# Kernel optimization log

Hardware: AMD Instinct MI355X
Metric: run time of the kernel (lower is better)

## Reference

```python
import jax, jax.numpy as jnp
import numpy as np

EPS = 1e-5

def _ln(t, w, b):
    m = t.mean(-1, keepdims=True)
    xc = t - m
    var = (xc * xc).mean(-1, keepdims=True)
    return xc * jax.lax.rsqrt(var + EPS) * w + b

def _rope(q, k, cos, sin):
    # q,k: [B,H,N,hd]; cos,sin: [N, hd//2]
    def rot(t):
        B, H, N, hd = t.shape
        tp = t.reshape(B, H, N, hd // 2, 2)
        r, i = tp[..., 0], tp[..., 1]
        c = cos[None, None, :, :]
        s = sin[None, None, :, :]
        orr = r * c - i * s
        oii = r * s + i * c
        return jnp.stack([orr, oii], axis=-1).reshape(B, H, N, hd)
    return rot(q), rot(k)

def setup_inputs() -> dict:
    key = jax.random.key(0)
    B, N1, N2, D, H = 2, 2048, 256, 1024, 16
    hd = D // H
    ks = jax.random.split(key, 8)
    def w(k, shape):
        return jax.random.normal(k, shape, jnp.float32) * 0.02
    x = jax.random.normal(ks[0], (B, N1, D), jnp.float32)
    c = jax.random.normal(ks[1], (B, N2, D), jnp.float32)
    # rotary tables
    t = jnp.arange(N1, dtype=jnp.float32)
    inv_freq = 1.0 / (10000.0 ** (jnp.arange(0, hd, 2, dtype=jnp.float32) / hd))
    ang = jnp.outer(t, inv_freq)  # [N1, hd//2]
    return dict(
        x=x, c=c,
        freqs_cos=jnp.cos(ang), freqs_sin=jnp.sin(ang),
        W_qkv1=w(ks[2], (D, 3 * D)), b_qkv1=jnp.zeros(3 * D, jnp.float32),
        W_qkv2=w(ks[3], (D, 3 * D)), b_qkv2=jnp.zeros(3 * D, jnp.float32),
        qn1_w=jnp.ones(hd, jnp.float32), qn1_b=jnp.zeros(hd, jnp.float32),
        kn1_w=jnp.ones(hd, jnp.float32), kn1_b=jnp.zeros(hd, jnp.float32),
        qn2_w=jnp.ones(hd, jnp.float32), qn2_b=jnp.zeros(hd, jnp.float32),
        kn2_w=jnp.ones(hd, jnp.float32), kn2_b=jnp.zeros(hd, jnp.float32),
        W_proj1=w(ks[4], (D, D)), b_proj1=jnp.zeros(D, jnp.float32),
        W_proj2=w(ks[5], (D, D)), b_proj2=jnp.zeros(D, jnp.float32),
        pre_x=0,
    )

def reference(x, c, freqs_cos, freqs_sin,
              W_qkv1, b_qkv1, W_qkv2, b_qkv2,
              qn1_w, qn1_b, kn1_w, kn1_b,
              qn2_w, qn2_b, kn2_w, kn2_b,
              W_proj1, b_proj1, W_proj2, b_proj2, pre_x):
    B, N1, D = x.shape
    N2 = c.shape[1]
    H = 16
    hd = D // H
    scale = hd ** -0.5

    def split_heads(qkv):
        q, k, v = jnp.split(qkv, 3, axis=-1)
        f = lambda t: t.reshape(B, -1, H, hd).transpose(0, 2, 1, 3)
        return f(q), f(k), f(v)

    q1, k1, v1 = split_heads(x @ W_qkv1 + b_qkv1)
    q1 = _ln(q1, qn1_w, qn1_b)
    k1 = _ln(k1, kn1_w, kn1_b)
    if pre_x:
        qr, kr = _rope(q1[:, :, pre_x:], k1[:, :, pre_x:], freqs_cos, freqs_sin)
        q1 = jnp.concatenate([q1[:, :, :pre_x], qr], axis=2)
        k1 = jnp.concatenate([k1[:, :, :pre_x], kr], axis=2)
    else:
        q1, k1 = _rope(q1, k1, freqs_cos, freqs_sin)

    q2, k2, v2 = split_heads(c @ W_qkv2 + b_qkv2)
    q2 = _ln(q2, qn2_w, qn2_b)
    k2 = _ln(k2, kn2_w, kn2_b)

    q = jnp.concatenate([q1, q2], axis=2)
    k = jnp.concatenate([k1, k2], axis=2)
    v = jnp.concatenate([v1, v2], axis=2)

    scores = jnp.einsum('bhqd,bhkd->bhqk', q, k) * scale
    attn = jax.nn.softmax(scores, axis=-1)
    o = jnp.einsum('bhqk,bhkd->bhqd', attn, v)  # [B,H,N,hd]
    o = o.transpose(0, 2, 1, 3).reshape(B, N1 + N2, D)

    x_out = o[:, :N1] @ W_proj1 + b_proj1
    c_out = o[:, N1:] @ W_proj2 + b_proj2
    return (x_out, c_out)
```

## Files before the change

kernel.cpp:

```cpp
#include <hip/hip_runtime.h>
#include <hip/hip_bf16.h>
#include <stdint.h>

typedef __attribute__((ext_vector_type(8))) short short8;
typedef __attribute__((ext_vector_type(4))) short bf4;
typedef __attribute__((ext_vector_type(4))) float f32x4;

#define B_ 2
#define N1 2048
#define N2 256
#define NT 2304
#define D_ 1024
#define H_ 16
#define HD 64
#define QSCALE 0.18033688011112042f
#define RESCALE_THR 8.0f

static __device__ __forceinline__ float bf2f(short s){
  union { unsigned int u; float f; } u;
  u.u = ((unsigned int)(unsigned short)s) << 16;
  return u.f;
}
static __device__ __forceinline__ short f2bf(float f){
  union { float f; unsigned int u; } v; v.f = f;
  unsigned int u = v.u;
  unsigned int lsb = (u >> 16) & 1u;
  u += 0x7fffu + lsb;
  return (short)(u >> 16);
}
static __device__ __forceinline__ unsigned int cvtpk2(float a, float b){
  union { __hip_bfloat162 h; unsigned int u; } cv;
  cv.h = __float22bfloat162_rn(make_float2(a, b));
  return cv.u;
}

static __device__ __forceinline__ float fexp2(float x){
#if __has_builtin(__builtin_amdgcn_exp2f)
  return __builtin_amdgcn_exp2f(x);
#else
  return exp2f(x);
#endif
}

static __device__ __forceinline__ void gload16(const void* g, void* l){
  __builtin_amdgcn_global_load_lds(
      (const __attribute__((address_space(1))) void*)g,
      (__attribute__((address_space(3))) void*)l, 16, 0, 0);
}

static __device__ __forceinline__ int swz(int row, int chunk){
  return (row << 6) + ((chunk ^ (row & 7)) << 3);
}

__global__ __launch_bounds__(256) void k_cvt_all(const float* __restrict__ x,
                                                 const float* __restrict__ c,
                                                 short* __restrict__ out){
  int i = (blockIdx.x * 256 + threadIdx.x) * 8;
  const float* in = (i < 4194304) ? (x + i) : (c + (i - 4194304));
  float4 a = *(const float4*)(in);
  float4 b = *(const float4*)(in + 4);
  short8 o;
  o[0]=f2bf(a.x); o[1]=f2bf(a.y); o[2]=f2bf(a.z); o[3]=f2bf(a.w);
  o[4]=f2bf(b.x); o[5]=f2bf(b.y); o[6]=f2bf(b.z); o[7]=f2bf(b.w);
  *(short8*)(out + i) = o;
}

__global__ __launch_bounds__(256) void k_transpose_w4(
    const float* __restrict__ Wq1, const float* __restrict__ Wq2,
    const float* __restrict__ Wp1, const float* __restrict__ Wp2,
    short* __restrict__ Wt1, short* __restrict__ Wt2,
    short* __restrict__ Wtp1, short* __restrict__ Wtp2){
  const int id = blockIdx.x;
  const float* W; short* Wt; int N; int bx, by;
  if (id < 768)      { W = Wq1; Wt = Wt1;  N = 3072; bx = id % 48;          by = id / 48; }
  else if (id < 1536){ W = Wq2; Wt = Wt2;  N = 3072; bx = (id-768) % 48;    by = (id-768) / 48; }
  else if (id < 1792){ W = Wp1; Wt = Wtp1; N = 1024; bx = (id-1536) % 16;   by = (id-1536) / 16; }
  else               { W = Wp2; Wt = Wtp2; N = 1024; bx = (id-1792) % 16;   by = (id-1792) / 16; }
  const int K = 1024;
  __shared__ float tl[64][65];
  const int n0 = bx * 64, k0 = by * 64;
  const int t = threadIdx.x, r = t >> 2, c = (t & 3) * 16;
  const float* src = W + (size_t)(k0 + r) * N + n0 + c;
  #pragma unroll
  for (int i = 0; i < 16; i += 4){
    float4 v = *(const float4*)(src + i);
    tl[r][c+i] = v.x; tl[r][c+i+1] = v.y; tl[r][c+i+2] = v.z; tl[r][c+i+3] = v.w;
  }
  __syncthreads();
  short8 o0, o1;
  #pragma unroll
  for (int i = 0; i < 8; i++) o0[i] = f2bf(tl[c+i][r]);
  #pragma unroll
  for (int i = 0; i < 8; i++) o1[i] = f2bf(tl[c+8+i][r]);
  short* dst = Wt + (size_t)(n0 + r) * K + k0 + c;
  *(short8*)(dst)     = o0;
  *(short8*)(dst + 8) = o1;
}

__global__ __launch_bounds__(256) void k_gemm_qkv(const short* __restrict__ A,
    const short* __restrict__ Bt, const short* __restrict__ Bt2,
    const float* __restrict__ bias, const float* __restrict__ bias2,
    const float* __restrict__ qn1w, const float* __restrict__ qn1b,
    const float* __restrict__ kn1w, const float* __restrict__ kn1b,
    const float* __restrict__ qn2w, const float* __restrict__ qn2b,
    const float* __restrict__ kn2w, const float* __restrict__ kn2b,
    const float* __restrict__ fcos, const float* __restrict__ fsin,
    short* __restrict__ Qo, short* __restrict__ Ko, short* __restrict__ Vto){
  __shared__ __align__(16) short As[128*32];
  __shared__ __align__(16) short Bs[128*32];
  const int t = threadIdx.x;
  const int w = t >> 6, l = t & 63;
  const int lc = l & 15, g = l >> 4;
  const int gx = gridDim.x;
  const int nb = gx * gridDim.y;
  const int bid = blockIdx.y * gx + blockIdx.x;
  const int nbid = (bid & 7) * (nb >> 3) + (bid >> 3);
  const int tm = (nbid / gx) * 128, tn = (nbid % gx) * 128;
  const int wm = (w >> 1) * 64, wn = (w & 1) * 64;
  const int K = 1024;
  const bool s1 = (tm < 4096);

  const short* Bsel = s1 ? Bt : Bt2;
  const float* bsel = s1 ? bias : bias2;

  const int r0 = w*32 + (l >> 2);
  const int r1 = r0 + 16;
  const int cb = (l & 3) * 16;

  const char* Ag0 = (const char*)(A + (size_t)(tm + r0) * K) + cb;
  const char* Ag1 = (const char*)(A + (size_t)(tm + r1) * K) + cb;
  const char* Bg0 = (const char*)(Bsel + (size_t)(tn + r0) * K) + cb;
  const char* Bg1 = (const char*)(Bsel + (size_t)(tn + r1) * K) + cb;
  char* Al0 = (char*)As + (w*2  )*1024;
  char* Al1 = (char*)As + (w*2+1)*1024;
  char* Bl0 = (char*)Bs + (w*2  )*1024;
  char* Bl1 = (char*)Bs + (w*2+1)*1024;

  f32x4 acc[4][4];
  #pragma unroll
  for (int m=0;m<4;m++){
    #pragma unroll
    for (int n=0;n<4;n++){ acc[m][n][0]=0.f; acc[m][n][1]=0.f; acc[m][n][2]=0.f; acc[m][n][3]=0.f; }
  }

  for (int k0 = 0; k0 < K; k0 += 32){
    const int kb = k0 * 2;
    gload16(Ag0 + kb, Al0);
    gload16(Ag1 + kb, Al1);
    gload16(Bg0 + kb, Bl0);
    gload16(Bg1 + kb, Bl1);
    __syncthreads();
    short8 af[4], bfr[4];
    #pragma unroll
    for (int m=0;m<4;m++) af[m]  = *(const short8*)(As + (wm + m*16 + lc)*32 + g*8);
    #pragma unroll
    for (int n=0;n<4;n++) bfr[n] = *(const short8*)(Bs + (wn + n*16 + lc)*32 + g*8);
    #pragma unroll
    for (int m=0;m<4;m++){
      #pragma unroll
      for (int n=0;n<4;n++)
        acc[m][n] = __builtin_amdgcn_mfma_f32_16x16x32_bf16(af[m], bfr[n], acc[m][n], 0, 0, 0);
    }
    __syncthreads();
  }

  #pragma unroll
  for (int n=0;n<4;n++){
    const float bv = bsel[tn + wn + n*16 + lc];
    #pragma unroll
    for (int m=0;m<4;m++){
      acc[m][n][0] += bv; acc[m][n][1] += bv; acc[m][n][2] += bv; acc[m][n][3] += bv;
    }
  }

  const int colbase = tn + wn;
  const int grp = colbase >> 10;
  const int hh = (colbase & 1023) >> 6;

  if (grp == 2){
    #pragma unroll
    for (int m=0;m<4;m++){
      const int row0 = tm + wm + m*16 + g*4;
      const int bb  = s1 ? (row0 >> 11) : ((row0 - 4096) >> 8);
      const int pos = s1 ? (row0 & 2047) : (2048 + ((row0 - 4096) & 255));
      short* vbase = Vto + (size_t)(bb*16 + hh) * 64 * NT + pos;
      #pragma unroll
      for (int n=0;n<4;n++){
        const int d = n*16 + lc;
        bf4 ov;
        #pragma unroll
        for (int r=0;r<4;r++) ov[r] = f2bf(acc[m][n][r]);
        *(bf4*)(vbase + (size_t)d * NT) = ov;
      }
    }
    return;
  }

  const float* lnw = (grp == 0) ? (s1 ? qn1w : qn2w) : (s1 ? kn1w : kn2w);
  const float* lnb = (grp == 0) ? (s1 ? qn1b : qn2b) : (s1 ? kn1b : kn2b);
  short* outp = (grp == 0) ? Qo : Ko;
  float wv_[4], bv_[4];
  #pragma unroll
  for (int n=0;n<4;n++){ wv_[n] = lnw[n*16 + lc]; bv_[n] = lnb[n*16 + lc]; }

  #pragma unroll
  for (int m=0;m<4;m++){
    float mu[4], rv[4];
    #pragma unroll
    for (int r=0;r<4;r++){
      float s  = (acc[m][0][r] + acc[m][1][r]) + (acc[m][2][r] + acc[m][3][r]);
      float sq = (acc[m][0][r]*acc[m][0][r] + acc[m][1][r]*acc[m][1][r])
               + (acc[m][2][r]*acc[m][2][r] + acc[m][3][r]*acc[m][3][r]);
      s  += __shfl_xor(s, 1, 64);  sq += __shfl_xor(sq, 1, 64);
      s  += __shfl_xor(s, 2, 64);  sq += __shfl_xor(sq, 2, 64);
      s  += __shfl_xor(s, 4, 64);  sq += __shfl_xor(sq, 4, 64);
      s  += __shfl_xor(s, 8, 64);  sq += __shfl_xor(sq, 8, 64);
      mu[r] = s * (1.f/64.f);
      const float var = sq * (1.f/64.f) - mu[r]*mu[r];
      rv[r] = rsqrtf(var + 1e-5f);
    }
    const int row0 = tm + wm + m*16 + g*4;
    const int bb  = s1 ? (row0 >> 11) : ((row0 - 4096) >> 8);
    const int pos0 = s1 ? (row0 & 2047) : (2048 + ((row0 - 4096) & 255));
    short* obase = outp + ((size_t)(bb*16 + hh) * NT + pos0) * 64;
    #pragma unroll
    for (int n=0;n<4;n++){
      float xh[4];
      #pragma unroll
      for (int r=0;r<4;r++) xh[r] = (acc[m][n][r] - mu[r]) * rv[r] * wv_[n] + bv_[n];
      if (s1){
        #pragma unroll
        for (int r=0;r<4;r++){
          const size_t fi = (size_t)(pos0 + r) * 32 + n*8 + (lc >> 1);
          const float cv = fcos[fi];
          const float sv = fsin[fi];
          const float p = __shfl_xor(xh[r], 1, 64);
          xh[r] = (lc & 1) ? (p*sv + xh[r]*cv) : (xh[r]*cv - p*sv);
        }
      }
      if (grp == 0){
        #pragma unroll
        for (int r=0;r<4;r++) xh[r] *= QSCALE;
      }
      const int d = n*16 + lc;
      #pragma unroll
      for (int r=0;r<4;r++) obase[(size_t)r * 64 + d] = f2bf(xh[r]);
    }
  }
}

__global__ __launch_bounds__(256) void k_gemm_proj(const short* __restrict__ A,
                                                   const short* __restrict__ Bt,
                                                   const short* __restrict__ Bt2,
                                                   const float* __restrict__ bias,
                                                   const float* __restrict__ bias2,
                                                   float* __restrict__ Cp,
                                                   int N, int K, int Msplit){
  __shared__ __align__(16) short As[128*32];
  __shared__ __align__(16) short Bs[128*32];
  const int t = threadIdx.x;
  const int w = t >> 6, l = t & 63;
  const int lc = l & 15, g = l >> 4;
  const int gx = gridDim.x;
  const int nb = gx * gridDim.y;
  const int bid = blockIdx.y * gx + blockIdx.x;
  const int nbid = (bid & 7) * (nb >> 3) + (bid >> 3);
  const int tm = (nbid / gx) * 128, tn = (nbid % gx) * 128;
  const int wm = (w >> 1) * 64, wn = (w & 1) * 64;

  const short* Bsel = (tm < Msplit) ? Bt : Bt2;
  const float* bsel = (tm < Msplit) ? bias : bias2;

  const int r0 = w*32 + (l >> 2);
  const int r1 = r0 + 16;
  const int cb = (l & 3) * 16;

  const char* Ag0 = (const char*)(A + (size_t)(tm + r0) * K) + cb;
  const char* Ag1 = (const char*)(A + (size_t)(tm + r1) * K) + cb;
  const char* Bg0 = (const char*)(Bsel + (size_t)(tn + r0) * K) + cb;
  const char* Bg1 = (const char*)(Bsel + (size_t)(tn + r1) * K) + cb;
  char* Al0 = (char*)As + (w*2  )*1024;
  char* Al1 = (char*)As + (w*2+1)*1024;
  char* Bl0 = (char*)Bs + (w*2  )*1024;
  char* Bl1 = (char*)Bs + (w*2+1)*1024;

  f32x4 acc[4][4];
  #pragma unroll
  for (int m=0;m<4;m++){
    #pragma unroll
    for (int n=0;n<4;n++){ acc[m][n][0]=0.f; acc[m][n][1]=0.f; acc[m][n][2]=0.f; acc[m][n][3]=0.f; }
  }

  for (int k0 = 0; k0 < K; k0 += 32){
    const int kb = k0 * 2;
    gload16(Ag0 + kb, Al0);
    gload16(Ag1 + kb, Al1);
    gload16(Bg0 + kb, Bl0);
    gload16(Bg1 + kb, Bl1);
    __syncthreads();
    short8 af[4], bfr[4];
    #pragma unroll
    for (int m=0;m<4;m++) af[m]  = *(const short8*)(As + (wm + m*16 + lc)*32 + g*8);
    #pragma unroll
    for (int n=0;n<4;n++) bfr[n] = *(const short8*)(Bs + (wn + n*16 + lc)*32 + g*8);
    #pragma unroll
    for (int m=0;m<4;m++){
      #pragma unroll
      for (int n=0;n<4;n++)
        acc[m][n] = __builtin_amdgcn_mfma_f32_16x16x32_bf16(af[m], bfr[n], acc[m][n], 0, 0, 0);
    }
    __syncthreads();
  }

  #pragma unroll
  for (int n=0;n<4;n++){
    const int col = tn + wn + n*16 + lc;
    const float bv = bsel[col];
    #pragma unroll
    for (int m=0;m<4;m++){
      const int row = tm + wm + m*16 + g*4;
      #pragma unroll
      for (int r=0;r<4;r++)
        Cp[(size_t)(row + r)*N + col] = acc[m][n][r] + bv;
    }
  }
}

__global__ __launch_bounds__(512) void k_attn(const short* __restrict__ Q,
                                              const short* __restrict__ Kg,
                                              const short* __restrict__ Vt,
                                              short* __restrict__ o1,
                                              short* __restrict__ o2){
  __shared__ __align__(16) short Kl[2][4096];
  __shared__ __align__(16) short Vl[2][4096];
  __shared__ __align__(16) short Ps[8][1024];
  const int t = threadIdx.x, w = t >> 6, l = t & 63;
  const int lc = l & 15, g = l >> 4;
  const int blk = blockIdx.x;
  const int ch = blk & 7, ii = blk >> 3;
  const int bh = ch * 4 + (ii / 18);
  const int qt = ii % 18;
  const int b = bh >> 4, hh = bh & 15;
  const int q0 = qt * 128 + w * 16;
  const short* Qb = Q  + (size_t)bh * NT * HD;
  const short* Kb = Kg + (size_t)bh * NT * HD;
  const short* Vb = Vt + (size_t)bh * HD * NT;

  short8 qf0 = *(const short8*)(Qb + (size_t)(q0 + lc) * HD + g*8);
  short8 qf1 = *(const short8*)(Qb + (size_t)(q0 + lc) * HD + g*8 + 32);

  const int sr = t >> 3, c0 = t & 7;
  const short* Kgp = Kb + (size_t)sr * HD + c0 * 8;
  const short* Vgp = Vb + (size_t)sr * NT + c0 * 8;
  const int w0 = swz(sr, c0);

  float mcur = -1e30f, lcur = 0.f;
  f32x4 oacc[4];
  #pragma unroll
  for (int j=0;j<4;j++){ oacc[j][0]=0.f; oacc[j][1]=0.f; oacc[j][2]=0.f; oacc[j][3]=0.f; }

  {
    short8 k0 = *(const short8*)(Kgp);
    short8 v0 = *(const short8*)(Vgp);
    *(short8*)&Kl[0][w0] = k0;
    *(short8*)&Vl[0][w0] = v0;
  }
  __syncthreads();

  for (int ti = 0; ti < 36; ++ti){
    const int cur = ti & 1;
    short8 kn0, vn0;
    if (ti < 35){
      kn0 = *(const short8*)(Kgp + (size_t)(ti + 1) * 64 * HD);
      vn0 = *(const short8*)(Vgp + (ti + 1) * 64);
    }
    f32x4 s[4];
    __builtin_amdgcn_s_setprio(1);
    #pragma unroll
    for (int j=0;j<4;j++){
      const int row = j*16 + lc;
      short8 k0 = *(const short8*)(&Kl[cur][swz(row, g)]);
      short8 k1 = *(const short8*)(&Kl[cur][swz(row, g + 4)]);
      f32x4 a; a[0]=0.f; a[1]=0.f; a[2]=0.f; a[3]=0.f;
      a = __builtin_amdgcn_mfma_f32_16x16x32_bf16(k0, qf0, a, 0, 0, 0);
      a = __builtin_amdgcn_mfma_f32_16x16x32_bf16(k1, qf1, a, 0, 0, 0);
      s[j] = a;
    }
    __builtin_amdgcn_s_setprio(0);
    float t0 = fmaxf(fmaxf(s[0][0], s[0][1]), fmaxf(s[0][2], s[0][3]));
    float t1 = fmaxf(fmaxf(s[1][0], s[1][1]), fmaxf(s[1][2], s[1][3]));
    float t2 = fmaxf(fmaxf(s[2][0], s[2][1]), fmaxf(s[2][2], s[2][3]));
    float t3 = fmaxf(fmaxf(s[3][0], s[3][1]), fmaxf(s[3][2], s[3][3]));
    float tmx = fmaxf(fmaxf(t0, t1), fmaxf(t2, t3));
    tmx = fmaxf(tmx, __shfl_xor(tmx, 16, 64));
    tmx = fmaxf(tmx, __shfl_xor(tmx, 32, 64));
    float mn = mcur;
    if (__any(tmx > mcur + RESCALE_THR)){
      mn = fmaxf(mcur, tmx);
      const float fsc = fexp2(mcur - mn);
      mcur = mn;
      lcur *= fsc;
      #pragma unroll
      for (int j=0;j<4;j++){
        oacc[j][0] *= fsc; oacc[j][1] *= fsc; oacc[j][2] *= fsc; oacc[j][3] *= fsc;
      }
    }
    float p[4][4];
    #pragma unroll
    for (int j=0;j<4;j++){
      p[j][0] = fexp2(s[j][0] - mn);
      p[j][1] = fexp2(s[j][1] - mn);
      p[j][2] = fexp2(s[j][2] - mn);
      p[j][3] = fexp2(s[j][3] - mn);
    }
    float rs = ((p[0][0]+p[0][1])+(p[0][2]+p[0][3]))
             + ((p[1][0]+p[1][1])+(p[1][2]+p[1][3]))
             + ((p[2][0]+p[2][1])+(p[2][2]+p[2][3]))
             + ((p[3][0]+p[3][1])+(p[3][2]+p[3][3]));
    rs += __shfl_xor(rs, 16, 64);
    rs += __shfl_xor(rs, 32, 64);
    lcur += rs;
    #pragma unroll
    for (int j=0;j<4;j++){
      const int si = (lc << 6) + (((2*j + (g >> 1)) ^ (lc & 7)) << 3) + (g & 1) * 4;
      unsigned int* dst = (unsigned int*)&Ps[w][si];
      dst[0] = cvtpk2(p[j][0], p[j][1]);
      dst[1] = cvtpk2(p[j][2], p[j][3]);
    }
    #pragma unroll
    for (int kk=0;kk<2;kk++){
      short8 pa = *(const short8*)(&Ps[w][swz(lc, 4*kk + g)]);
      __builtin_amdgcn_s_setprio(1);
      #pragma unroll
      for (int jd=0;jd<4;jd++){
        short8 vb = *(const short8*)(&Vl[cur][swz(lc + 16*jd, 4*kk + g)]);
        oacc[jd] = __builtin_amdgcn_mfma_f32_16x16x32_bf16(vb, pa, oacc[jd], 0, 0, 0);
      }
      __builtin_amdgcn_s_setprio(0);
    }
    if (ti < 35){
      *(short8*)&Kl[cur ^ 1][w0] = kn0;
      *(short8*)&Vl[cur ^ 1][w0] = vn0;
    }
    __syncthreads();
  }

  const float inv = 1.0f / lcur;
  const int qi = q0 + lc;
  short* obase = (qi < N1) ? (o1 + ((size_t)b * N1 + qi) * D_)
                           : (o2 + ((size_t)b * N2 + (qi - N1)) * D_);
  #pragma unroll
  for (int jd=0;jd<4;jd++){
    bf4 ov;
    #pragma unroll
    for (int r=0;r<4;r++) ov[r] = f2bf(oacc[jd][r] * inv);
    *(bf4*)(obase + hh*64 + 16*jd + 4*g) = ov;
  }
}

extern "C" void kernel_launch(void* const* d_in, const int* in_sizes, int n_in,
                              void* d_out, int out_size, void* d_ws, size_t ws_size,
                              hipStream_t stream){
  const float* x    = (const float*)d_in[0];
  const float* c    = (const float*)d_in[1];
  const float* fc   = (const float*)d_in[2];
  const float* fs   = (const float*)d_in[3];
  const float* Wq1  = (const float*)d_in[4];
  const float* bq1  = (const float*)d_in[5];
  const float* Wq2  = (const float*)d_in[6];
  const float* bq2  = (const float*)d_in[7];
  const float* qn1w = (const float*)d_in[8];
  const float* qn1b = (const float*)d_in[9];
  const float* kn1w = (const float*)d_in[10];
  const float* kn1b = (const float*)d_in[11];
  const float* qn2w = (const float*)d_in[12];
  const float* qn2b = (const float*)d_in[13];
  const float* kn2w = (const float*)d_in[14];
  const float* kn2b = (const float*)d_in[15];
  const float* Wp1  = (const float*)d_in[16];
  const float* bp1  = (const float*)d_in[17];
  const float* Wp2  = (const float*)d_in[18];
  const float* bp2  = (const float*)d_in[19];
  float* out = (float*)d_out;

  char* ws = (char*)d_ws;
  short* xb   = (short*)(ws);
  short* Wt1  = (short*)(ws + 9437184);
  short* Wt2  = (short*)(ws + 15728640);
  short* Wtp1 = (short*)(ws + 22020096);
  short* Wtp2 = (short*)(ws + 24117248);
  short* o1   = (short*)(ws + 26214400);
  short* Vtb  = (short*)(ws + 26214400 + 9437184);
  short* Qb   = (short*)(ws + 54525952);
  short* Kb   = (short*)(ws + 63963136);

  k_cvt_all<<<2304, 256, 0, stream>>>(x, c, xb);
  k_transpose_w4<<<2048, 256, 0, stream>>>(Wq1, Wq2, Wp1, Wp2, Wt1, Wt2, Wtp1, Wtp2);

  k_gemm_qkv<<<dim3(24,36), 256, 0, stream>>>(xb, Wt1, Wt2, bq1, bq2,
      qn1w, qn1b, kn1w, kn1b, qn2w, qn2b, kn2w, kn2b, fc, fs, Qb, Kb, Vtb);

  k_attn<<<576, 512, 0, stream>>>(Qb, Kb, Vtb, o1, o1 + 4194304);

  k_gemm_proj<<<dim3(8,36), 256, 0, stream>>>(o1, Wtp1, Wtp2, bp1, bp2, out, 1024, 1024, 4096);
}
```

Measured before the change: 189.4 us.

## Process two query tiles per warp in attention with 256-thread blocks

Attention blocks drop from 8 to 4 warps, and each warp now handles two 16-row query tiles against the same K/V fragments. Each K and V fragment read from shared memory feeds two MFMAs, which halves LDS reads per unit of compute and adds independent work per warp. The cost is roughly double the accumulator and softmax registers per thread and fewer waves per block, which may lower occupancy and latency hiding.

```diff
diff --git a/kernel.cpp b/kernel.cpp
--- a/kernel.cpp
+++ b/kernel.cpp
@@ -326,14 +326,14 @@
   }
 }
 
-__global__ __launch_bounds__(512) void k_attn(const short* __restrict__ Q,
+__global__ __launch_bounds__(256) void k_attn(const short* __restrict__ Q,
                                               const short* __restrict__ Kg,
                                               const short* __restrict__ Vt,
                                               short* __restrict__ o1,
                                               short* __restrict__ o2){
   __shared__ __align__(16) short Kl[2][4096];
   __shared__ __align__(16) short Vl[2][4096];
-  __shared__ __align__(16) short Ps[8][1024];
+  __shared__ __align__(16) short Ps[4][2][1024];
   const int t = threadIdx.x, w = t >> 6, l = t & 63;
   const int lc = l & 15, g = l >> 4;
   const int blk = blockIdx.x;
@@ -346,35 +346,48 @@
   const short* Kb = Kg + (size_t)bh * NT * HD;
   const short* Vb = Vt + (size_t)bh * HD * NT;
 
-  short8 qf0 = *(const short8*)(Qb + (size_t)(q0 + lc) * HD + g*8);
-  short8 qf1 = *(const short8*)(Qb + (size_t)(q0 + lc) * HD + g*8 + 32);
-
-  const int sr = t >> 3, c0 = t & 7;
+  short8 qA0 = *(const short8*)(Qb + (size_t)(q0 + lc) * HD + g*8);
+  short8 qA1 = *(const short8*)(Qb + (size_t)(q0 + lc) * HD + g*8 + 32);
+  short8 qB0 = *(const short8*)(Qb + (size_t)(q0 + 64 + lc) * HD + g*8);
+  short8 qB1 = *(const short8*)(Qb + (size_t)(q0 + 64 + lc) * HD + g*8 + 32);
+
+  const int sr = t >> 2, c0 = (t & 3) * 2;
   const short* Kgp = Kb + (size_t)sr * HD + c0 * 8;
   const short* Vgp = Vb + (size_t)sr * NT + c0 * 8;
-  const int w0 = swz(sr, c0);
-
-  float mcur = -1e30f, lcur = 0.f;
-  f32x4 oacc[4];
-  #pragma unroll
-  for (int j=0;j<4;j++){ oacc[j][0]=0.f; oacc[j][1]=0.f; oacc[j][2]=0.f; oacc[j][3]=0.f; }
+  const int w0 = swz(sr, c0), w1 = swz(sr, c0 + 1);
+
+  float mA = -1e30f, lA = 0.f, mB = -1e30f, lB = 0.f;
+  f32x4 oA[4], oB[4];
+  #pragma unroll
+  for (int j=0;j<4;j++){
+    oA[j][0]=0.f; oA[j][1]=0.f; oA[j][2]=0.f; oA[j][3]=0.f;
+    oB[j][0]=0.f; oB[j][1]=0.f; oB[j][2]=0.f; oB[j][3]=0.f;
+  }
 
   {
     short8 k0 = *(const short8*)(Kgp);
+    short8 k1 = *(const short8*)(Kgp + 8);
     short8 v0 = *(const short8*)(Vgp);
+    short8 v1 = *(const short8*)(Vgp + 8);
     *(short8*)&Kl[0][w0] = k0;
+    *(short8*)&Kl[0][w1] = k1;
     *(short8*)&Vl[0][w0] = v0;
+    *(short8*)&Vl[0][w1] = v1;
   }
   __syncthreads();
 
   for (int ti = 0; ti < 36; ++ti){
     const int cur = ti & 1;
-    short8 kn0, vn0;
+    short8 kn0, kn1, vn0, vn1;
     if (ti < 35){
-      kn0 = *(const short8*)(Kgp + (size_t)(ti + 1) * 64 * HD);
-      vn0 = *(const short8*)(Vgp + (ti + 1) * 64);
-    }
-    f32x4 s[4];
+      const short* kp = Kgp + (size_t)(ti + 1) * 64 * HD;
+      const short* vp = Vgp + (ti + 1) * 64;
+      kn0 = *(const short8*)(kp);
+      kn1 = *(const short8*)(kp + 8);
+      vn0 = *(const short8*)(vp);
+      vn1 = *(const short8*)(vp + 8);
+    }
+    f32x4 sA[4], sB[4];
     __builtin_amdgcn_s_setprio(1);
     #pragma unroll
     for (int j=0;j<4;j++){
@@ -382,79 +395,147 @@
       short8 k0 = *(const short8*)(&Kl[cur][swz(row, g)]);
       short8 k1 = *(const short8*)(&Kl[cur][swz(row, g + 4)]);
       f32x4 a; a[0]=0.f; a[1]=0.f; a[2]=0.f; a[3]=0.f;
-      a = __builtin_amdgcn_mfma_f32_16x16x32_bf16(k0, qf0, a, 0, 0, 0);
-      a = __builtin_amdgcn_mfma_f32_16x16x32_bf16(k1, qf1, a, 0, 0, 0);
-      s[j] = a;
+      a = __builtin_amdgcn_mfma_f32_16x16x32_bf16(k0, qA0, a, 0, 0, 0);
+      a = __builtin_amdgcn_mfma_f32_16x16x32_bf16(k1, qA1, a, 0, 0, 0);
+      sA[j] = a;
+      f32x4 bb; bb[0]=0.f; bb[1]=0.f; bb[2]=0.f; bb[3]=0.f;
+      bb = __builtin_amdgcn_mfma_f32_16x16x32_bf16(k0, qB0, bb, 0, 0, 0);
+      bb = __builtin_amdgcn_mfma_f32_16x16x32_bf16(k1, qB1, bb, 0, 0, 0);
+      sB[j] = bb;
     }
     __builtin_amdgcn_s_setprio(0);
-    float t0 = fmaxf(fmaxf(s[0][0], s[0][1]), fmaxf(s[0][2], s[0][3]));
-    float t1 = fmaxf(fmaxf(s[1][0], s[1][1]), fmaxf(s[1][2], s[1][3]));
-    float t2 = fmaxf(fmaxf(s[2][0], s[2][1]), fmaxf(s[2][2], s[2][3]));
-    float t3 = fmaxf(fmaxf(s[3][0], s[3][1]), fmaxf(s[3][2], s[3][3]));
-    float tmx = fmaxf(fmaxf(t0, t1), fmaxf(t2, t3));
-    tmx = fmaxf(tmx, __shfl_xor(tmx, 16, 64));
-    tmx = fmaxf(tmx, __shfl_xor(tmx, 32, 64));
-    float mn = mcur;
-    if (__any(tmx > mcur + RESCALE_THR)){
-      mn = fmaxf(mcur, tmx);
-      const float fsc = fexp2(mcur - mn);
-      mcur = mn;
-      lcur *= fsc;
+
+    {
+      float t0 = fmaxf(fmaxf(sA[0][0], sA[0][1]), fmaxf(sA[0][2], sA[0][3]));
+      float t1 = fmaxf(fmaxf(sA[1][0], sA[1][1]), fmaxf(sA[1][2], sA[1][3]));
+      float t2 = fmaxf(fmaxf(sA[2][0], sA[2][1]), fmaxf(sA[2][2], sA[2][3]));
+      float t3 = fmaxf(fmaxf(sA[3][0], sA[3][1]), fmaxf(sA[3][2], sA[3][3]));
+      float tmx = fmaxf(fmaxf(t0, t1), fmaxf(t2, t3));
+      tmx = fmaxf(tmx, __shfl_xor(tmx, 16, 64));
+      tmx = fmaxf(tmx, __shfl_xor(tmx, 32, 64));
+      float mn = mA;
+      if (__any(tmx > mA + RESCALE_THR)){
+        mn = fmaxf(mA, tmx);
+        const float fsc = fexp2(mA - mn);
+        mA = mn;
+        lA *= fsc;
+        #pragma unroll
+        for (int j=0;j<4;j++){
+          oA[j][0] *= fsc; oA[j][1] *= fsc; oA[j][2] *= fsc; oA[j][3] *= fsc;
+        }
+      }
+      float p[4][4];
       #pragma unroll
       for (int j=0;j<4;j++){
-        oacc[j][0] *= fsc; oacc[j][1] *= fsc; oacc[j][2] *= fsc; oacc[j][3] *= fsc;
-      }
-    }
-    float p[4][4];
-    #pragma unroll
-    for (int j=0;j<4;j++){
-      p[j][0] = fexp2(s[j][0] - mn);
-      p[j][1] = fexp2(s[j][1] - mn);
-      p[j][2] = fexp2(s[j][2] - mn);
-      p[j][3] = fexp2(s[j][3] - mn);
-    }
-    float rs = ((p[0][0]+p[0][1])+(p[0][2]+p[0][3]))
-             + ((p[1][0]+p[1][1])+(p[1][2]+p[1][3]))
-             + ((p[2][0]+p[2][1])+(p[2][2]+p[2][3]))
-             + ((p[3][0]+p[3][1])+(p[3][2]+p[3][3]));
-    rs += __shfl_xor(rs, 16, 64);
-    rs += __shfl_xor(rs, 32, 64);
-    lcur += rs;
-    #pragma unroll
-    for (int j=0;j<4;j++){
-      const int si = (lc << 6) + (((2*j + (g >> 1)) ^ (lc & 7)) << 3) + (g & 1) * 4;
-      unsigned int* dst = (unsigned int*)&Ps[w][si];
-      dst[0] = cvtpk2(p[j][0], p[j][1]);
-      dst[1] = cvtpk2(p[j][2], p[j][3]);
+        p[j][0] = fexp2(sA[j][0] - mn);
+        p[j][1] = fexp2(sA[j][1] - mn);
+        p[j][2] = fexp2(sA[j][2] - mn);
+        p[j][3] = fexp2(sA[j][3] - mn);
+      }
+      float rs = ((p[0][0]+p[0][1])+(p[0][2]+p[0][3]))
+               + ((p[1][0]+p[1][1])+(p[1][2]+p[1][3]))
+               + ((p[2][0]+p[2][1])+(p[2][2]+p[2][3]))
+               + ((p[3][0]+p[3][1])+(p[3][2]+p[3][3]));
+      rs += __shfl_xor(rs, 16, 64);
+      rs += __shfl_xor(rs, 32, 64);
+      lA += rs;
+      #pragma unroll
+      for (int j=0;j<4;j++){
+        const int si = (lc << 6) + (((2*j + (g >> 1)) ^ (lc & 7)) << 3) + (g & 1) * 4;
+        unsigned int* dst = (unsigned int*)&Ps[w][0][si];
+        dst[0] = cvtpk2(p[j][0], p[j][1]);
+        dst[1] = cvtpk2(p[j][2], p[j][3]);
+      }
+    }
+    {
+      float t0 = fmaxf(fmaxf(sB[0][0], sB[0][1]), fmaxf(sB[0][2], sB[0][3]));
+      float t1 = fmaxf(fmaxf(sB[1][0], sB[1][1]), fmaxf(sB[1][2], sB[1][3]));
+      float t2 = fmaxf(fmaxf(sB[2][0], sB[2][1]), fmaxf(sB[2][2], sB[2][3]));
+      float t3 = fmaxf(fmaxf(sB[3][0], sB[3][1]), fmaxf(sB[3][2], sB[3][3]));
+      float tmx = fmaxf(fmaxf(t0, t1), fmaxf(t2, t3));
+      tmx = fmaxf(tmx, __shfl_xor(tmx, 16, 64));
+      tmx = fmaxf(tmx, __shfl_xor(tmx, 32, 64));
+      float mn = mB;
+      if (__any(tmx > mB + RESCALE_THR)){
+        mn = fmaxf(mB, tmx);
+        const float fsc = fexp2(mB - mn);
+        mB = mn;
+        lB *= fsc;
+        #pragma unroll
+        for (int j=0;j<4;j++){
+          oB[j][0] *= fsc; oB[j][1] *= fsc; oB[j][2] *= fsc; oB[j][3] *= fsc;
+        }
+      }
+      float p[4][4];
+      #pragma unroll
+      for (int j=0;j<4;j++){
+        p[j][0] = fexp2(sB[j][0] - mn);
+        p[j][1] = fexp2(sB[j][1] - mn);
+        p[j][2] = fexp2(sB[j][2] - mn);
+        p[j][3] = fexp2(sB[j][3] - mn);
+      }
+      float rs = ((p[0][0]+p[0][1])+(p[0][2]+p[0][3]))
+               + ((p[1][0]+p[1][1])+(p[1][2]+p[1][3]))
+               + ((p[2][0]+p[2][1])+(p[2][2]+p[2][3]))
+               + ((p[3][0]+p[3][1])+(p[3][2]+p[3][3]));
+      rs += __shfl_xor(rs, 16, 64);
+      rs += __shfl_xor(rs, 32, 64);
+      lB += rs;
+      #pragma unroll
+      for (int j=0;j<4;j++){
+        const int si = (lc << 6) + (((2*j + (g >> 1)) ^ (lc & 7)) << 3) + (g & 1) * 4;
+        unsigned int* dst = (unsigned int*)&Ps[w][1][si];
+        dst[0] = cvtpk2(p[j][0], p[j][1]);
+        dst[1] = cvtpk2(p[j][2], p[j][3]);
+      }
     }
     #pragma unroll
     for (int kk=0;kk<2;kk++){
-      short8 pa = *(const short8*)(&Ps[w][swz(lc, 4*kk + g)]);
+      short8 paA = *(const short8*)(&Ps[w][0][swz(lc, 4*kk + g)]);
+      short8 paB = *(const short8*)(&Ps[w][1][swz(lc, 4*kk + g)]);
       __builtin_amdgcn_s_setprio(1);
       #pragma unroll
       for (int jd=0;jd<4;jd++){
         short8 vb = *(const short8*)(&Vl[cur][swz(lc + 16*jd, 4*kk + g)]);
-        oacc[jd] = __builtin_amdgcn_mfma_f32_16x16x32_bf16(vb, pa, oacc[jd], 0, 0, 0);
+        oA[jd] = __builtin_amdgcn_mfma_f32_16x16x32_bf16(vb, paA, oA[jd], 0, 0, 0);
+        oB[jd] = __builtin_amdgcn_mfma_f32_16x16x32_bf16(vb, paB, oB[jd], 0, 0, 0);
       }
       __builtin_amdgcn_s_setprio(0);
     }
     if (ti < 35){
       *(short8*)&Kl[cur ^ 1][w0] = kn0;
+      *(short8*)&Kl[cur ^ 1][w1] = kn1;
       *(short8*)&Vl[cur ^ 1][w0] = vn0;
+      *(short8*)&Vl[cur ^ 1][w1] = vn1;
     }
     __syncthreads();
   }
 
-  const float inv = 1.0f / lcur;
-  const int qi = q0 + lc;
-  short* obase = (qi < N1) ? (o1 + ((size_t)b * N1 + qi) * D_)
-                           : (o2 + ((size_t)b * N2 + (qi - N1)) * D_);
-  #pragma unroll
-  for (int jd=0;jd<4;jd++){
-    bf4 ov;
-    #pragma unroll
-    for (int r=0;r<4;r++) ov[r] = f2bf(oacc[jd][r] * inv);
-    *(bf4*)(obase + hh*64 + 16*jd + 4*g) = ov;
+  {
+    const float inv = 1.0f / lA;
+    const int qi = q0 + lc;
+    short* obase = (qi < N1) ? (o1 + ((size_t)b * N1 + qi) * D_)
+                             : (o2 + ((size_t)b * N2 + (qi - N1)) * D_);
+    #pragma unroll
+    for (int jd=0;jd<4;jd++){
+      bf4 ov;
+      #pragma unroll
+      for (int r=0;r<4;r++) ov[r] = f2bf(oA[jd][r] * inv);
+      *(bf4*)(obase + hh*64 + 16*jd + 4*g) = ov;
+    }
+  }
+  {
+    const float inv = 1.0f / lB;
+    const int qi = q0 + 64 + lc;
+    short* obase = (qi < N1) ? (o1 + ((size_t)b * N1 + qi) * D_)
+                             : (o2 + ((size_t)b * N2 + (qi - N1)) * D_);
+    #pragma unroll
+    for (int jd=0;jd<4;jd++){
+      bf4 ov;
+      #pragma unroll
+      for (int r=0;r<4;r++) ov[r] = f2bf(oB[jd][r] * inv);
+      *(bf4*)(obase + hh*64 + 16*jd + 4*g) = ov;
+    }
   }
 }
 
@@ -500,7 +581,7 @@
   k_gemm_qkv<<<dim3(24,36), 256, 0, stream>>>(xb, Wt1, Wt2, bq1, bq2,
       qn1w, qn1b, kn1w, kn1b, qn2w, qn2b, kn2w, kn2b, fc, fs, Qb, Kb, Vtb);
 
-  k_attn<<<576, 512, 0, stream>>>(Qb, Kb, Vtb, o1, o1 + 4194304);
+  k_attn<<<576, 256, 0, stream>>>(Qb, Kb, Vtb, o1, o1 + 4194304);
 
   k_gemm_proj<<<dim3(8,36), 256, 0, stream>>>(o1, Wtp1, Wtp2, bp1, bp2, out, 1024, 1024, 4096);
 }
```

New measurement: 218.4 us. 1.15x slower.

## Rework attention kernel around 32x32 MFMA with register-resident P and direct LDS loads

Applied to the files above, without the earlier changes.

Rewrites the attention kernel to run 4 waves of 32 query rows each, using 32x32x16 bf16 MFMA for both QK^T and PV. The softmax probabilities stay in registers and are reshuffled across the two wave halves with lane shuffles, which removes the per-wave LDS staging buffer. K and V tiles now go straight from global memory into LDS through pre-swizzled global_load_lds, and the swizzle function gains an extra XOR term. The intent is to cut LDS traffic, shuffle and reduction work per tile and to raise MFMA efficiency. In exchange each thread holds more accumulator registers and the block has half as many threads.

```diff
diff --git a/kernel.cpp b/kernel.cpp
--- a/kernel.cpp
+++ b/kernel.cpp
@@ -5,6 +5,7 @@
 typedef __attribute__((ext_vector_type(8))) short short8;
 typedef __attribute__((ext_vector_type(4))) short bf4;
 typedef __attribute__((ext_vector_type(4))) float f32x4;
+typedef __attribute__((ext_vector_type(16))) float f32x16;
 
 #define B_ 2
 #define N1 2048
@@ -49,7 +50,7 @@
 }
 
 static __device__ __forceinline__ int swz(int row, int chunk){
-  return (row << 6) + ((chunk ^ (row & 7)) << 3);
+  return (row << 6) + (((chunk ^ (row & 7) ^ ((row >> 3) & 7)) & 7) << 3);
 }
 
 __global__ __launch_bounds__(256) void k_cvt_all(const float* __restrict__ x,
@@ -326,73 +327,85 @@
   }
 }
 
-__global__ __launch_bounds__(512) void k_attn(const short* __restrict__ Q,
+__global__ __launch_bounds__(256) void k_attn(const short* __restrict__ Q,
                                               const short* __restrict__ Kg,
                                               const short* __restrict__ Vt,
                                               short* __restrict__ o1,
                                               short* __restrict__ o2){
   __shared__ __align__(16) short Kl[2][4096];
   __shared__ __align__(16) short Vl[2][4096];
-  __shared__ __align__(16) short Ps[8][1024];
   const int t = threadIdx.x, w = t >> 6, l = t & 63;
-  const int lc = l & 15, g = l >> 4;
+  const int q32 = l & 31, h5 = l >> 5;
   const int blk = blockIdx.x;
   const int ch = blk & 7, ii = blk >> 3;
   const int bh = ch * 4 + (ii / 18);
   const int qt = ii % 18;
   const int b = bh >> 4, hh = bh & 15;
-  const int q0 = qt * 128 + w * 16;
+  const int qrow = qt*128 + w*32 + q32;
   const short* Qb = Q  + (size_t)bh * NT * HD;
   const short* Kb = Kg + (size_t)bh * NT * HD;
   const short* Vb = Vt + (size_t)bh * HD * NT;
 
-  short8 qf0 = *(const short8*)(Qb + (size_t)(q0 + lc) * HD + g*8);
-  short8 qf1 = *(const short8*)(Qb + (size_t)(q0 + lc) * HD + g*8 + 32);
-
-  const int sr = t >> 3, c0 = t & 7;
-  const short* Kgp = Kb + (size_t)sr * HD + c0 * 8;
-  const short* Vgp = Vb + (size_t)sr * NT + c0 * 8;
-  const int w0 = swz(sr, c0);
+  short8 qf[4];
+  #pragma unroll
+  for (int hk=0;hk<4;hk++)
+    qf[hk] = *(const short8*)(Qb + (size_t)qrow * HD + hk*16 + h5*8);
+
+  const int srow0 = w*16 + (l >> 3);
+  const int srow1 = srow0 + 8;
+  const int cg0 = (l & 7) ^ (srow0 & 7) ^ ((srow0 >> 3) & 7);
+  const int cg1 = (l & 7) ^ (srow1 & 7) ^ ((srow1 >> 3) & 7);
+  const short* Kg0 = Kb + (size_t)srow0 * HD + cg0*8;
+  const short* Kg1 = Kb + (size_t)srow1 * HD + cg1*8;
+  const short* Vg0 = Vb + (size_t)srow0 * NT + cg0*8;
+  const short* Vg1 = Vb + (size_t)srow1 * NT + cg1*8;
+  const int ld0 = w*1024, ld1 = w*1024 + 512;
 
   float mcur = -1e30f, lcur = 0.f;
-  f32x4 oacc[4];
-  #pragma unroll
-  for (int j=0;j<4;j++){ oacc[j][0]=0.f; oacc[j][1]=0.f; oacc[j][2]=0.f; oacc[j][3]=0.f; }
-
-  {
-    short8 k0 = *(const short8*)(Kgp);
-    short8 v0 = *(const short8*)(Vgp);
-    *(short8*)&Kl[0][w0] = k0;
-    *(short8*)&Vl[0][w0] = v0;
-  }
+  f32x16 oacc[2];
+  #pragma unroll
+  for (int db=0;db<2;db++){
+    #pragma unroll
+    for (int r=0;r<16;r++) oacc[db][r] = 0.f;
+  }
+
+  gload16(Kg0, (char*)&Kl[0][ld0]);
+  gload16(Kg1, (char*)&Kl[0][ld1]);
+  gload16(Vg0, (char*)&Vl[0][ld0]);
+  gload16(Vg1, (char*)&Vl[0][ld1]);
   __syncthreads();
 
-  for (int ti = 0; ti < 36; ++ti){
-    const int cur = ti & 1;
-    short8 kn0, vn0;
-    if (ti < 35){
-      kn0 = *(const short8*)(Kgp + (size_t)(ti + 1) * 64 * HD);
-      vn0 = *(const short8*)(Vgp + (ti + 1) * 64);
-    }
-    f32x4 s[4];
+  for (int pi = 0; pi < 36; ++pi){
+    const int cur = pi & 1;
+    if (pi < 35){
+      const size_t ko = (size_t)(pi + 1) * 64 * HD;
+      const int vo = (pi + 1) * 64;
+      gload16(Kg0 + ko, (char*)&Kl[cur ^ 1][ld0]);
+      gload16(Kg1 + ko, (char*)&Kl[cur ^ 1][ld1]);
+      gload16(Vg0 + vo, (char*)&Vl[cur ^ 1][ld0]);
+      gload16(Vg1 + vo, (char*)&Vl[cur ^ 1][ld1]);
+    }
+    f32x16 s[2];
     __builtin_amdgcn_s_setprio(1);
     #pragma unroll
-    for (int j=0;j<4;j++){
-      const int row = j*16 + lc;
-      short8 k0 = *(const short8*)(&Kl[cur][swz(row, g)]);
-      short8 k1 = *(const short8*)(&Kl[cur][swz(row, g + 4)]);
-      f32x4 a; a[0]=0.f; a[1]=0.f; a[2]=0.f; a[3]=0.f;
-      a = __builtin_amdgcn_mfma_f32_16x16x32_bf16(k0, qf0, a, 0, 0, 0);
-      a = __builtin_amdgcn_mfma_f32_16x16x32_bf16(k1, qf1, a, 0, 0, 0);
-      s[j] = a;
+    for (int kvb=0;kvb<2;kvb++){
+      f32x16 a;
+      #pragma unroll
+      for (int r=0;r<16;r++) a[r] = 0.f;
+      #pragma unroll
+      for (int hk=0;hk<4;hk++){
+        short8 kf = *(const short8*)(&Kl[cur][swz(kvb*32 + q32, hk*2 + h5)]);
+        a = __builtin_amdgcn_mfma_f32_32x32x16_bf16(kf, qf[hk], a, 0, 0, 0);
+      }
+      s[kvb] = a;
     }
     __builtin_amdgcn_s_setprio(0);
-    float t0 = fmaxf(fmaxf(s[0][0], s[0][1]), fmaxf(s[0][2], s[0][3]));
-    float t1 = fmaxf(fmaxf(s[1][0], s[1][1]), fmaxf(s[1][2], s[1][3]));
-    float t2 = fmaxf(fmaxf(s[2][0], s[2][1]), fmaxf(s[2][2], s[2][3]));
-    float t3 = fmaxf(fmaxf(s[3][0], s[3][1]), fmaxf(s[3][2], s[3][3]));
-    float tmx = fmaxf(fmaxf(t0, t1), fmaxf(t2, t3));
-    tmx = fmaxf(tmx, __shfl_xor(tmx, 16, 64));
+    float tmx = -1e30f;
+    #pragma unroll
+    for (int kvb=0;kvb<2;kvb++){
+      #pragma unroll
+      for (int r=0;r<16;r++) tmx = fmaxf(tmx, s[kvb][r]);
+    }
     tmx = fmaxf(tmx, __shfl_xor(tmx, 32, 64));
     float mn = mcur;
     if (__any(tmx > mcur + RESCALE_THR)){
@@ -401,60 +414,62 @@
       mcur = mn;
       lcur *= fsc;
       #pragma unroll
-      for (int j=0;j<4;j++){
-        oacc[j][0] *= fsc; oacc[j][1] *= fsc; oacc[j][2] *= fsc; oacc[j][3] *= fsc;
-      }
-    }
-    float p[4][4];
-    #pragma unroll
-    for (int j=0;j<4;j++){
-      p[j][0] = fexp2(s[j][0] - mn);
-      p[j][1] = fexp2(s[j][1] - mn);
-      p[j][2] = fexp2(s[j][2] - mn);
-      p[j][3] = fexp2(s[j][3] - mn);
-    }
-    float rs = ((p[0][0]+p[0][1])+(p[0][2]+p[0][3]))
-             + ((p[1][0]+p[1][1])+(p[1][2]+p[1][3]))
-             + ((p[2][0]+p[2][1])+(p[2][2]+p[2][3]))
-             + ((p[3][0]+p[3][1])+(p[3][2]+p[3][3]));
-    rs += __shfl_xor(rs, 16, 64);
+      for (int db=0;db<2;db++){
+        #pragma unroll
+        for (int r=0;r<16;r++) oacc[db][r] *= fsc;
+      }
+    }
+    float rs = 0.f;
+    #pragma unroll
+    for (int kvb=0;kvb<2;kvb++){
+      #pragma unroll
+      for (int r=0;r<16;r++){
+        s[kvb][r] = fexp2(s[kvb][r] - mn);
+        rs += s[kvb][r];
+      }
+    }
     rs += __shfl_xor(rs, 32, 64);
     lcur += rs;
     #pragma unroll
-    for (int j=0;j<4;j++){
-      const int si = (lc << 6) + (((2*j + (g >> 1)) ^ (lc & 7)) << 3) + (g & 1) * 4;
-      unsigned int* dst = (unsigned int*)&Ps[w][si];
-      dst[0] = cvtpk2(p[j][0], p[j][1]);
-      dst[1] = cvtpk2(p[j][2], p[j][3]);
-    }
-    #pragma unroll
-    for (int kk=0;kk<2;kk++){
-      short8 pa = *(const short8*)(&Ps[w][swz(lc, 4*kk + g)]);
+    for (int kvs=0;kvs<4;kvs++){
+      const int kvb = kvs >> 1, sb = kvs & 1;
+      const unsigned int A0 = cvtpk2(s[kvb][8*sb+0], s[kvb][8*sb+1]);
+      const unsigned int A1 = cvtpk2(s[kvb][8*sb+2], s[kvb][8*sb+3]);
+      const unsigned int B0 = cvtpk2(s[kvb][8*sb+4], s[kvb][8*sb+5]);
+      const unsigned int B1 = cvtpk2(s[kvb][8*sb+6], s[kvb][8*sb+7]);
+      const unsigned int X0 = (unsigned int)__shfl_xor((int)A0, 32, 64);
+      const unsigned int X1 = (unsigned int)__shfl_xor((int)A1, 32, 64);
+      const unsigned int Y0 = (unsigned int)__shfl_xor((int)B0, 32, 64);
+      const unsigned int Y1 = (unsigned int)__shfl_xor((int)B1, 32, 64);
+      union { unsigned int u[4]; short8 s8; } pf;
+      pf.u[0] = h5 ? Y0 : A0;
+      pf.u[1] = h5 ? Y1 : A1;
+      pf.u[2] = h5 ? B0 : X0;
+      pf.u[3] = h5 ? B1 : X1;
       __builtin_amdgcn_s_setprio(1);
       #pragma unroll
-      for (int jd=0;jd<4;jd++){
-        short8 vb = *(const short8*)(&Vl[cur][swz(lc + 16*jd, 4*kk + g)]);
-        oacc[jd] = __builtin_amdgcn_mfma_f32_16x16x32_bf16(vb, pa, oacc[jd], 0, 0, 0);
+      for (int db=0;db<2;db++){
+        short8 vf = *(const short8*)(&Vl[cur][swz(db*32 + q32, kvs*2 + h5)]);
+        oacc[db] = __builtin_amdgcn_mfma_f32_32x32x16_bf16(vf, pf.s8, oacc[db], 0, 0, 0);
       }
       __builtin_amdgcn_s_setprio(0);
     }
-    if (ti < 35){
-      *(short8*)&Kl[cur ^ 1][w0] = kn0;
-      *(short8*)&Vl[cur ^ 1][w0] = vn0;
-    }
     __syncthreads();
   }
 
   const float inv = 1.0f / lcur;
-  const int qi = q0 + lc;
+  const int qi = qrow;
   short* obase = (qi < N1) ? (o1 + ((size_t)b * N1 + qi) * D_)
                            : (o2 + ((size_t)b * N2 + (qi - N1)) * D_);
   #pragma unroll
-  for (int jd=0;jd<4;jd++){
-    bf4 ov;
-    #pragma unroll
-    for (int r=0;r<4;r++) ov[r] = f2bf(oacc[jd][r] * inv);
-    *(bf4*)(obase + hh*64 + 16*jd + 4*g) = ov;
+  for (int db=0;db<2;db++){
+    #pragma unroll
+    for (int rg=0;rg<4;rg++){
+      bf4 ov;
+      #pragma unroll
+      for (int i=0;i<4;i++) ov[i] = f2bf(oacc[db][rg*4 + i] * inv);
+      *(bf4*)(obase + hh*64 + db*32 + rg*8 + h5*4) = ov;
+    }
   }
 }
 
@@ -500,7 +515,7 @@
   k_gemm_qkv<<<dim3(24,36), 256, 0, stream>>>(xb, Wt1, Wt2, bq1, bq2,
       qn1w, qn1b, kn1w, kn1b, qn2w, qn2b, kn2w, kn2b, fc, fs, Qb, Kb, Vtb);
 
-  k_attn<<<576, 512, 0, stream>>>(Qb, Kb, Vtb, o1, o1 + 4194304);
+  k_attn<<<576, 256, 0, stream>>>(Qb, Kb, Vtb, o1, o1 + 4194304);
 
   k_gemm_proj<<<dim3(8,36), 256, 0, stream>>>(o1, Wtp1, Wtp2, bp1, bp2, out, 1024, 1024, 4096);
 }
```

New measurement: 223.8 us. 1.18x slower.
